# Performance work log

Measured on AMD Instinct MI355X. Metric: run time of the kernel, lower is better.

The kernel has to match this reference:

```python
import jax, jax.numpy as jnp
import numpy as np

H, W = 256, 256
SIGMA = 1.5
INV_VAR = 1.0 / (2.0 * (SIGMA ** 2 + 1e-08))

def setup_inputs() -> dict:
    key = jax.random.key(0)
    k1, k2 = jax.random.split(key)
    B, K, N = 4, 8, 4096
    # pixel-coordinate points, slightly over-ranged to test edge behavior
    points_2d = jax.random.uniform(k1, (B, K, N, 2), dtype=jnp.float32,
                                   minval=-4.0, maxval=260.0)
    points_z = jax.random.uniform(k2, (B, K, N), dtype=jnp.float32,
                                  minval=0.0, maxval=5.0)
    return {"points_2d": points_2d, "points_z": points_z}

def reference(points_2d, points_z):
    # points_2d: (B, K, N, 2); points_z: (B, K, N)
    x = points_2d[..., 0]                      # (B,K,N)
    y = points_2d[..., 1]                      # (B,K,N)
    xg = jnp.arange(W, dtype=points_2d.dtype)  # (W,)
    yg = jnp.arange(H, dtype=points_2d.dtype)  # (H,)
    # Separable Gaussian: exp(-(dx^2+dy^2)*c) = exp(-dx^2*c) * exp(-dy^2*c)
    wx = jnp.exp(-((xg - x[..., None]) ** 2) * INV_VAR)  # (B,K,N,W)
    wy = jnp.exp(-((yg - y[..., None]) ** 2) * INV_VAR)  # (B,K,N,H)
    inv_z = 1.0 / jnp.clip(points_z, 1e-05, None)        # (B,K,N)
    wy = wy * inv_z[..., None]
    # sum over points of outer products -> (B,K,H,W)
    return jnp.einsum('bknh,bknw->bkhw', wy, wx)
```

## Files before the change

kernel.cpp:

```cpp
#include <hip/hip_runtime.h>
#include <hip/hip_bf16.h>

typedef __attribute__((ext_vector_type(8))) short bf16x8;
typedef __attribute__((ext_vector_type(4))) float f32x4;
typedef __attribute__((ext_vector_type(4))) unsigned int u32x4;

constexpr int BM = 32;
constexpr int BN = 32;
constexpr int BK = 32;
constexpr int NPTS = 4096;
constexpr int HH = 256;
constexpr int WW = 256;
constexpr int SEGCAP = 128;

#define SCALE_S 0.56621453f
#define DCUT 10.0f

__device__ inline unsigned int pkbf(float a, float b) {
    unsigned ua = __builtin_bit_cast(unsigned, a);
    unsigned ub = __builtin_bit_cast(unsigned, b);
    return ((ua + 0x8000u) >> 16) | ((ub + 0x8000u) & 0xFFFF0000u);
}

__global__ __launch_bounds__(256, 8) void soft_raster_kernel(
    const float* __restrict__ p2d,
    const float* __restrict__ pz,
    float* __restrict__ out)
{
    const int bk  = blockIdx.z;
    const int tm  = blockIdx.y * BM;
    const int tn  = blockIdx.x * BN;
    const int tid = threadIdx.x;

    __shared__ __align__(16) unsigned short lwy[BM * BK];
    __shared__ __align__(16) unsigned short lwx[BN * BK];
    __shared__ unsigned short lidx[4 * SEGCAP];
    __shared__ int scnt[4];
    __shared__ float lys[BK];
    __shared__ float lxs[BK];
    __shared__ float lzi[BK];

    const int wid  = tid >> 6;
    const int lane = tid & 63;
    const int wm   = (wid >> 1) << 4;
    const int wn   = (wid & 1) << 4;
    const int g    = lane >> 4;
    const int r    = lane & 15;

    const size_t pbase = (size_t)bk * NPTS;
    const float2* __restrict__ pxy = reinterpret_cast<const float2*>(p2d) + pbase;

    const float xlo = (float)tn - DCUT, xhi = (float)(tn + BN - 1) + DCUT;
    const float ylo = (float)tm - DCUT, yhi = (float)(tm + BM - 1) + DCUT;

    int base = 0;
    #pragma unroll 4
    for (int it = 0; it < 16; ++it) {
        const int k = (wid << 10) + (it << 6) + lane;
        float2 xy = pxy[k];
        bool in = (xy.x > xlo) && (xy.x < xhi) && (xy.y > ylo) && (xy.y < yhi);
        unsigned long long b = __ballot(in);
        int pos = __popcll(b & ((1ull << lane) - 1ull));
        if (in && (base + pos) < SEGCAP)
            lidx[(wid << 7) + base + pos] = (unsigned short)k;
        base += __popcll(b);
    }
    if (lane == 0) scnt[wid] = (base < SEGCAP) ? base : SEGCAP;
    __syncthreads();

    const int c0 = scnt[0], c1 = scnt[1], c2 = scnt[2], c3 = scnt[3];
    const int p1 = c0, p2 = c0 + c1, p3 = c0 + c1 + c2;
    const int total = p3 + c3;

    f32x4 acc = {};

    for (int k0 = 0; k0 < total; k0 += BK) {
        __syncthreads();

        if (tid < BK) {
            const int j = k0 + tid;
            float xs = 0.f, ys = 0.f, zi = -__builtin_inff();
            if (j < total) {
                const int seg = (j >= p1) + (j >= p2) + (j >= p3);
                const int off = (seg > 0) ? ((seg > 1) ? ((seg > 2) ? p3 : p2) : p1) : 0;
                const int kk  = lidx[(seg << 7) + (j - off)];
                float2 xy = pxy[kk];
                float  z  = pz[pbase + kk];
                xs = xy.x * SCALE_S;
                ys = xy.y * SCALE_S;
                zi = -__builtin_amdgcn_logf(fmaxf(z, 1e-5f));
            }
            lxs[tid] = xs; lys[tid] = ys; lzi[tid] = zi;
        }
        __syncthreads();

        {
            const bool isy = (tid < 128);
            const float* coord  = isy ? lys : lxs;
            unsigned short* dst = isy ? lwy : lwx;
            const int cb        = isy ? tm  : tn;
            const int cc = tid & 127;
            const int q  = cc >> 2;
            const int kg = cc & 3;
            const float qs = (float)(cb + q) * SCALE_S;
            float4 c0v = *reinterpret_cast<const float4*>(&coord[kg * 8]);
            float4 c1v = *reinterpret_cast<const float4*>(&coord[kg * 8 + 4]);
            float m0 = 0.f, m1 = 0.f, m2 = 0.f, m3 = 0.f;
            float m4 = 0.f, m5 = 0.f, m6 = 0.f, m7 = 0.f;
            if (isy) {
                float4 z0 = *reinterpret_cast<const float4*>(&lzi[kg * 8]);
                float4 z1 = *reinterpret_cast<const float4*>(&lzi[kg * 8 + 4]);
                m0 = z0.x; m1 = z0.y; m2 = z0.z; m3 = z0.w;
                m4 = z1.x; m5 = z1.y; m6 = z1.z; m7 = z1.w;
            }
            const float d0 = qs - c0v.x, d1 = qs - c0v.y, d2 = qs - c0v.z, d3 = qs - c0v.w;
            const float d4 = qs - c1v.x, d5 = qs - c1v.y, d6 = qs - c1v.z, d7 = qs - c1v.w;
            const float e0 = __builtin_amdgcn_exp2f(fmaf(d0, -d0, m0));
            const float e1 = __builtin_amdgcn_exp2f(fmaf(d1, -d1, m1));
            const float e2 = __builtin_amdgcn_exp2f(fmaf(d2, -d2, m2));
            const float e3 = __builtin_amdgcn_exp2f(fmaf(d3, -d3, m3));
            const float e4 = __builtin_amdgcn_exp2f(fmaf(d4, -d4, m4));
            const float e5 = __builtin_amdgcn_exp2f(fmaf(d5, -d5, m5));
            const float e6 = __builtin_amdgcn_exp2f(fmaf(d6, -d6, m6));
            const float e7 = __builtin_amdgcn_exp2f(fmaf(d7, -d7, m7));
            u32x4 v;
            v[0] = pkbf(e0, e1); v[1] = pkbf(e2, e3);
            v[2] = pkbf(e4, e5); v[3] = pkbf(e6, e7);
            *reinterpret_cast<u32x4*>(&dst[(q << 5) + (kg << 3)]) = v;
        }
        __syncthreads();

        {
            bf16x8 af = *reinterpret_cast<const bf16x8*>(
                &lwy[((wm + r) << 5) + (g << 3)]);
            bf16x8 bfr = *reinterpret_cast<const bf16x8*>(
                &lwx[((wn + r) << 5) + (g << 3)]);
            acc = __builtin_amdgcn_mfma_f32_16x16x32_bf16(af, bfr, acc, 0, 0, 0);
        }
    }

    float* obase = out + (size_t)bk * (HH * WW);
    const int col  = tn + wn + r;
    const int row0 = tm + wm + (g << 2);
    #pragma unroll
    for (int j = 0; j < 4; ++j)
        obase[(size_t)(row0 + j) * WW + col] = acc[j];
}

extern "C" void kernel_launch(void* const* d_in, const int* in_sizes, int n_in,
                              void* d_out, int out_size, void* d_ws, size_t ws_size,
                              hipStream_t stream) {
    const float* p2d = (const float*)d_in[0];
    const float* pz  = (const float*)d_in[1];
    float* out       = (float*)d_out;
    const int nbk    = in_sizes[1] / NPTS;
    dim3 grid(WW / BN, HH / BM, nbk);
    dim3 block(256);
    hipLaunchKernelGGL(soft_raster_kernel, grid, block, 0, stream, p2d, pz, out);
}
```

Before: 18.52 us.

## Compute Gaussian weights directly in MFMA registers, dropping per-chunk LDS staging

```diff
diff --git a/kernel.cpp b/kernel.cpp
--- a/kernel.cpp
+++ b/kernel.cpp
@@ -12,14 +12,15 @@
 constexpr int HH = 256;
 constexpr int WW = 256;
 constexpr int SEGCAP = 128;
+constexpr int CCAP = 4 * SEGCAP + BK;
 
 #define SCALE_S 0.56621453f
 #define DCUT 10.0f
 
-__device__ inline unsigned int pkbf(float a, float b) {
-    unsigned ua = __builtin_bit_cast(unsigned, a);
-    unsigned ub = __builtin_bit_cast(unsigned, b);
-    return ((ua + 0x8000u) >> 16) | ((ub + 0x8000u) & 0xFFFF0000u);
+__device__ inline unsigned cvtpk(float lo, float hi) {
+    unsigned r;
+    asm("v_cvt_pk_bf16_f32 %0, %1, %2" : "=v"(r) : "v"(lo), "v"(hi));
+    return r;
 }
 
 __global__ __launch_bounds__(256, 8) void soft_raster_kernel(
@@ -32,13 +33,9 @@
     const int tn  = blockIdx.x * BN;
     const int tid = threadIdx.x;
 
-    __shared__ __align__(16) unsigned short lwy[BM * BK];
-    __shared__ __align__(16) unsigned short lwx[BN * BK];
-    __shared__ unsigned short lidx[4 * SEGCAP];
+    __shared__ float sxs[4 * SEGCAP], sys[4 * SEGCAP], szi[4 * SEGCAP];
+    __shared__ __align__(16) float cxs[CCAP], cys[CCAP], czi[CCAP];
     __shared__ int scnt[4];
-    __shared__ float lys[BK];
-    __shared__ float lxs[BK];
-    __shared__ float lzi[BK];
 
     const int wid  = tid >> 6;
     const int lane = tid & 63;
@@ -61,8 +58,13 @@
         bool in = (xy.x > xlo) && (xy.x < xhi) && (xy.y > ylo) && (xy.y < yhi);
         unsigned long long b = __ballot(in);
         int pos = __popcll(b & ((1ull << lane) - 1ull));
-        if (in && (base + pos) < SEGCAP)
-            lidx[(wid << 7) + base + pos] = (unsigned short)k;
+        const int o = base + pos;
+        if (in && o < SEGCAP) {
+            const int s = (wid << 7) + o;
+            sxs[s] = xy.x * SCALE_S;
+            sys[s] = xy.y * SCALE_S;
+            szi[s] = -__builtin_amdgcn_logf(fmaxf(pz[pbase + k], 1e-5f));
+        }
         base += __popcll(b);
     }
     if (lane == 0) scnt[wid] = (base < SEGCAP) ? base : SEGCAP;
@@ -72,71 +74,61 @@
     const int p1 = c0, p2 = c0 + c1, p3 = c0 + c1 + c2;
     const int total = p3 + c3;
 
+    for (int j = tid; j < total + BK; j += 256) {
+        if (j < total) {
+            const int seg = (j >= p1) + (j >= p2) + (j >= p3);
+            const int off = (seg == 0) ? 0 : (seg == 1) ? p1 : (seg == 2) ? p2 : p3;
+            const int s   = (seg << 7) + (j - off);
+            cxs[j] = sxs[s]; cys[j] = sys[s]; czi[j] = szi[s];
+        } else {
+            cxs[j] = 0.f; cys[j] = 0.f; czi[j] = -__builtin_inff();
+        }
+    }
+    __syncthreads();
+
     f32x4 acc = {};
+    const float qy = (float)(tm + wm + r) * SCALE_S;
+    const float qx = (float)(tn + wn + r) * SCALE_S;
 
     for (int k0 = 0; k0 < total; k0 += BK) {
-        __syncthreads();
+        const int kb = k0 + (g << 3);
 
-        if (tid < BK) {
-            const int j = k0 + tid;
-            float xs = 0.f, ys = 0.f, zi = -__builtin_inff();
-            if (j < total) {
-                const int seg = (j >= p1) + (j >= p2) + (j >= p3);
-                const int off = (seg > 0) ? ((seg > 1) ? ((seg > 2) ? p3 : p2) : p1) : 0;
-                const int kk  = lidx[(seg << 7) + (j - off)];
-                float2 xy = pxy[kk];
-                float  z  = pz[pbase + kk];
-                xs = xy.x * SCALE_S;
-                ys = xy.y * SCALE_S;
-                zi = -__builtin_amdgcn_logf(fmaxf(z, 1e-5f));
-            }
-            lxs[tid] = xs; lys[tid] = ys; lzi[tid] = zi;
-        }
-        __syncthreads();
+        float4 y0 = *reinterpret_cast<const float4*>(&cys[kb]);
+        float4 y1 = *reinterpret_cast<const float4*>(&cys[kb + 4]);
+        float4 z0 = *reinterpret_cast<const float4*>(&czi[kb]);
+        float4 z1 = *reinterpret_cast<const float4*>(&czi[kb + 4]);
 
-        {
-            const bool isy = (tid < 128);
-            const float* coord  = isy ? lys : lxs;
-            unsigned short* dst = isy ? lwy : lwx;
-            const int cb        = isy ? tm  : tn;
-            const int cc = tid & 127;
-            const int q  = cc >> 2;
-            const int kg = cc & 3;
-            const float qs = (float)(cb + q) * SCALE_S;
-            float4 c0v = *reinterpret_cast<const float4*>(&coord[kg * 8]);
-            float4 c1v = *reinterpret_cast<const float4*>(&coord[kg * 8 + 4]);
-            float m0 = 0.f, m1 = 0.f, m2 = 0.f, m3 = 0.f;
-            float m4 = 0.f, m5 = 0.f, m6 = 0.f, m7 = 0.f;
-            if (isy) {
-                float4 z0 = *reinterpret_cast<const float4*>(&lzi[kg * 8]);
-                float4 z1 = *reinterpret_cast<const float4*>(&lzi[kg * 8 + 4]);
-                m0 = z0.x; m1 = z0.y; m2 = z0.z; m3 = z0.w;
-                m4 = z1.x; m5 = z1.y; m6 = z1.z; m7 = z1.w;
-            }
-            const float d0 = qs - c0v.x, d1 = qs - c0v.y, d2 = qs - c0v.z, d3 = qs - c0v.w;
-            const float d4 = qs - c1v.x, d5 = qs - c1v.y, d6 = qs - c1v.z, d7 = qs - c1v.w;
-            const float e0 = __builtin_amdgcn_exp2f(fmaf(d0, -d0, m0));
-            const float e1 = __builtin_amdgcn_exp2f(fmaf(d1, -d1, m1));
-            const float e2 = __builtin_amdgcn_exp2f(fmaf(d2, -d2, m2));
-            const float e3 = __builtin_amdgcn_exp2f(fmaf(d3, -d3, m3));
-            const float e4 = __builtin_amdgcn_exp2f(fmaf(d4, -d4, m4));
-            const float e5 = __builtin_amdgcn_exp2f(fmaf(d5, -d5, m5));
-            const float e6 = __builtin_amdgcn_exp2f(fmaf(d6, -d6, m6));
-            const float e7 = __builtin_amdgcn_exp2f(fmaf(d7, -d7, m7));
-            u32x4 v;
-            v[0] = pkbf(e0, e1); v[1] = pkbf(e2, e3);
-            v[2] = pkbf(e4, e5); v[3] = pkbf(e6, e7);
-            *reinterpret_cast<u32x4*>(&dst[(q << 5) + (kg << 3)]) = v;
-        }
-        __syncthreads();
+        float d;
+        u32x4 au;
+        d = qy - y0.x; const float a0 = __builtin_amdgcn_exp2f(fmaf(d, -d, z0.x));
+        d = qy - y0.y; const float a1 = __builtin_amdgcn_exp2f(fmaf(d, -d, z0.y));
+        d = qy - y0.z; const float a2 = __builtin_amdgcn_exp2f(fmaf(d, -d, z0.z));
+        d = qy - y0.w; const float a3 = __builtin_amdgcn_exp2f(fmaf(d, -d, z0.w));
+        d = qy - y1.x; const float a4 = __builtin_amdgcn_exp2f(fmaf(d, -d, z1.x));
+        d = qy - y1.y; const float a5 = __builtin_amdgcn_exp2f(fmaf(d, -d, z1.y));
+        d = qy - y1.z; const float a6 = __builtin_amdgcn_exp2f(fmaf(d, -d, z1.z));
+        d = qy - y1.w; const float a7 = __builtin_amdgcn_exp2f(fmaf(d, -d, z1.w));
+        au[0] = cvtpk(a0, a1); au[1] = cvtpk(a2, a3);
+        au[2] = cvtpk(a4, a5); au[3] = cvtpk(a6, a7);
 
-        {
-            bf16x8 af = *reinterpret_cast<const bf16x8*>(
-                &lwy[((wm + r) << 5) + (g << 3)]);
-            bf16x8 bfr = *reinterpret_cast<const bf16x8*>(
-                &lwx[((wn + r) << 5) + (g << 3)]);
-            acc = __builtin_amdgcn_mfma_f32_16x16x32_bf16(af, bfr, acc, 0, 0, 0);
-        }
+        float4 x0 = *reinterpret_cast<const float4*>(&cxs[kb]);
+        float4 x1 = *reinterpret_cast<const float4*>(&cxs[kb + 4]);
+
+        u32x4 bu;
+        d = qx - x0.x; const float b0 = __builtin_amdgcn_exp2f(-(d * d));
+        d = qx - x0.y; const float b1 = __builtin_amdgcn_exp2f(-(d * d));
+        d = qx - x0.z; const float b2 = __builtin_amdgcn_exp2f(-(d * d));
+        d = qx - x0.w; const float b3 = __builtin_amdgcn_exp2f(-(d * d));
+        d = qx - x1.x; const float b4 = __builtin_amdgcn_exp2f(-(d * d));
+        d = qx - x1.y; const float b5 = __builtin_amdgcn_exp2f(-(d * d));
+        d = qx - x1.z; const float b6 = __builtin_amdgcn_exp2f(-(d * d));
+        d = qx - x1.w; const float b7 = __builtin_amdgcn_exp2f(-(d * d));
+        bu[0] = cvtpk(b0, b1); bu[1] = cvtpk(b2, b3);
+        bu[2] = cvtpk(b4, b5); bu[3] = cvtpk(b6, b7);
+
+        acc = __builtin_amdgcn_mfma_f32_16x16x32_bf16(
+            __builtin_bit_cast(bf16x8, au), __builtin_bit_cast(bf16x8, bu),
+            acc, 0, 0, 0);
     }
 
     float* obase = out + (size_t)bk * (HH * WW);
```

New measurement: 18.91 us. 2.1% more time.
